# Optimization experiments

Measured on AMD Instinct MI355X. Metric: run time of the kernel, lower is better.

Reference implementation:

```python
import jax, jax.numpy as jnp
import numpy as np

N_NODES = 100000
M_EDGES = 500000
D = 128
L = 2
LRELU_SLOPE = 0.01
LN_EPS = 1e-5


def layer_norm(x, g, b):
    mu = jnp.mean(x, axis=-1, keepdims=True)
    var = jnp.var(x, axis=-1, keepdims=True)
    return (x - mu) * jax.lax.rsqrt(var + LN_EPS) * g + b


def leaky_relu(x):
    return jnp.where(x >= 0, x, LRELU_SLOPE * x)


def setup_inputs() -> dict:
    key = jax.random.key(0)
    ks = jax.random.split(key, 12)
    s = 1.0 / np.sqrt(D)
    inp = {
        "H": jax.random.normal(ks[0], (N_NODES, D), jnp.float32),
        "E": jax.random.normal(ks[1], (M_EDGES, D), jnp.float32),
        "ht": jax.random.randint(ks[2], (M_EDGES, 2), 0, N_NODES, jnp.int64) if jax.config.jax_enable_x64 else jax.random.randint(ks[2], (M_EDGES, 2), 0, N_NODES).astype(jnp.int32),
        "queries": jax.random.randint(ks[3], (M_EDGES,), 0, 2).astype(jnp.int32),
        # per-layer params stacked on leading L axis
        "W_eu": jax.random.uniform(ks[4], (L, 3 * D, D), jnp.float32, -s, s),
        "b_eu": jnp.zeros((L, D), jnp.float32),
        "ln_e_g": jnp.ones((L, D), jnp.float32),
        "ln_e_b": jnp.zeros((L, D), jnp.float32),
        "W_fwd": jax.random.uniform(ks[5], (L, 2 * D, D), jnp.float32, -s, s),
        "b_fwd": jnp.zeros((L, D), jnp.float32),
        "W_back": jax.random.uniform(ks[6], (L, 2 * D, D), jnp.float32, -s, s),
        "b_back": jnp.zeros((L, D), jnp.float32),
        "ln_h_g": jnp.ones((L, D), jnp.float32),
        "ln_h_b": jnp.zeros((L, D), jnp.float32),
    }
    return inp


def aggregate_messages(ht, messages_fwd, messages_back, n):
    # destinations: fwd msgs go to tails, back msgs go to heads
    msg_dst = jnp.concatenate([ht[:, 1], ht[:, 0]])  # [2m]
    messages = jnp.concatenate([messages_fwd, messages_back], axis=0)  # [2m, d]
    agg = jax.ops.segment_sum(messages, msg_dst, num_segments=n)  # [n, d]
    counts = jax.ops.segment_sum(jnp.ones_like(msg_dst, jnp.float32), msg_dst, num_segments=n)
    # torch yields nan/inf for count-0 nodes; clamp to 1 (0/1 = 0) for stability
    return agg / jnp.maximum(counts, 1.0)[:, None]


def reference(H, E, ht, queries, W_eu, b_eu, ln_e_g, ln_e_b,
              W_fwd, b_fwd, W_back, b_back, ln_h_g, ln_h_b):
    n = H.shape[0]
    for l in range(L):
        # --- EdgeUpdateLayer ---
        head_rep = H[ht[:, 0]]  # [m, d]
        tail_rep = H[ht[:, 1]]  # [m, d]
        triple = jnp.concatenate([head_rep, E, tail_rep], axis=1)  # [m, 3d]
        eu = leaky_relu(triple @ W_eu[l] + b_eu[l])
        E = layer_norm(eu + E, ln_e_g[l], ln_e_b[l])
        # --- MessagePassingLayer ---
        msgs_fwd = jnp.concatenate([H[ht[:, 0]], E], axis=1) @ W_fwd[l] + b_fwd[l]
        msgs_back = jnp.concatenate([H[ht[:, 1]], E], axis=1) @ W_back[l] + b_back[l]
        agg = aggregate_messages(ht, msgs_fwd, msgs_back, n)
        H = layer_norm(leaky_relu(agg) + H, ln_h_g[l], ln_h_b[l])
    return H
```

## Files before the change

### kernel.cpp

```cpp
#include <hip/hip_runtime.h>

#define N_NODES 100000
#define M_EDGES 500000
#define D 128
#define SLOPE 0.01f
#define EPS 1e-5f

typedef __attribute__((ext_vector_type(8))) short bf16x8;
typedef __attribute__((ext_vector_type(4))) float f32x4;
typedef __attribute__((ext_vector_type(4))) unsigned int u32x4;

__device__ __forceinline__ unsigned short f2bf(float f) {
    union { float f; unsigned u; } v; v.f = f;
    unsigned r = v.u + 0x7FFF + ((v.u >> 16) & 1);
    return (unsigned short)(r >> 16);
}
__device__ __forceinline__ float bf2f(unsigned short u) {
    union { unsigned u; float f; } v; v.u = ((unsigned)u) << 16; return v.f;
}
__device__ __forceinline__ u32x4 pack8v(f32x4 a, f32x4 b) {
    u32x4 r;
    r.x = ((unsigned)f2bf(a.y) << 16) | f2bf(a.x);
    r.y = ((unsigned)f2bf(a.w) << 16) | f2bf(a.z);
    r.z = ((unsigned)f2bf(b.y) << 16) | f2bf(b.x);
    r.w = ((unsigned)f2bf(b.w) << 16) | f2bf(b.z);
    return r;
}

__global__ void wconv_kernel(const float* __restrict__ src, unsigned short* __restrict__ dst,
                             int K, int total)
{
    int i = blockIdx.x * 256 + threadIdx.x;
    if (i >= total) return;
    int layer_sz = K * 128;
    int l = i / layer_sz;
    int r = i - l * layer_sz;
    int j    = r & 7;
    int lane = (r >> 3) & 63;
    int nt   = (r >> 9) & 7;
    int kk   = r >> 12;
    int row  = kk * 32 + ((lane >> 4) << 3) + j;
    int col  = nt * 16 + (lane & 15);
    dst[i] = f2bf(src[(size_t)l * layer_sz + row * 128 + col]);
}

__global__ void h2b_kernel(const float* __restrict__ src, unsigned short* __restrict__ dst, int total8)
{
    int i = blockIdx.x * 256 + threadIdx.x;
    if (i >= total8) return;
    f32x4 a = ((const f32x4*)src)[2 * i];
    f32x4 b = ((const f32x4*)src)[2 * i + 1];
    ((u32x4*)dst)[i] = pack8v(a, b);
}

__global__ void count_kernel(const int* __restrict__ ht, int* __restrict__ cnt, int m)
{
    int e = blockIdx.x * 256 + threadIdx.x;
    if (e < m) {
        atomicAdd(&cnt[ht[2 * e]],     1);
        atomicAdd(&cnt[ht[2 * e + 1]], 1);
    }
}

__global__ void scanA_kernel(const int* __restrict__ cnt, int* __restrict__ partial,
                             int* __restrict__ bsum, int n)
{
    __shared__ int tmp[256];
    int t = threadIdx.x, i = blockIdx.x * 256 + t;
    int v = (i < n) ? cnt[i] : 0;
    tmp[t] = v;
    __syncthreads();
    for (int s = 1; s < 256; s <<= 1) {
        int x = (t >= s) ? tmp[t - s] : 0;
        __syncthreads();
        tmp[t] += x;
        __syncthreads();
    }
    if (i < n) partial[i] = tmp[t] - v;
    if (t == 255) bsum[blockIdx.x] = tmp[255];
}

__global__ void scanB_kernel(int* __restrict__ bsum, int nb)
{
    __shared__ int tmp[512];
    int t = threadIdx.x;
    int v = (t < nb) ? bsum[t] : 0;
    tmp[t] = v;
    __syncthreads();
    for (int s = 1; s < 512; s <<= 1) {
        int x = (t >= s) ? tmp[t - s] : 0;
        __syncthreads();
        tmp[t] += x;
        __syncthreads();
    }
    if (t < nb) bsum[t] = tmp[t] - v;
}

__global__ void scanC_kernel(const int* __restrict__ partial, const int* __restrict__ bsum,
                             int* __restrict__ off, int* __restrict__ pos, int n)
{
    int i = blockIdx.x * 256 + threadIdx.x;
    if (i < n) {
        int o = partial[i] + bsum[blockIdx.x];
        off[i] = o;
        pos[i] = o;
    }
    if (i == 0) off[n] = 2 * M_EDGES;
}

__global__ void fill_kernel(const int* __restrict__ ht, int* __restrict__ pos,
                            int* __restrict__ slotF, int* __restrict__ slotB, int m)
{
    int e = blockIdx.x * 256 + threadIdx.x;
    if (e < m) {
        int2 p = ((const int2*)ht)[e];
        slotF[e] = atomicAdd(&pos[p.y], 1);
        slotB[e] = atomicAdd(&pos[p.x], 1);
    }
}

template <bool E_F32, bool WRITE_E>
__global__ __launch_bounds__(64, 2)
void edge_mfma_kernel(const unsigned short* __restrict__ Hb,
                      const float* __restrict__ E0,
                      const unsigned short* __restrict__ Ebf,
                      unsigned short* __restrict__ Eout,
                      const int* __restrict__ ht,
                      const unsigned short* __restrict__ Weu,
                      const unsigned short* __restrict__ Wf,
                      const unsigned short* __restrict__ Wb,
                      const float* __restrict__ beu,
                      const float* __restrict__ lneg, const float* __restrict__ lneb,
                      const float* __restrict__ bfw, const float* __restrict__ bbw,
                      const int* __restrict__ slotF, const int* __restrict__ slotB,
                      unsigned short* __restrict__ msg)
{
    __shared__ unsigned char en[16384];

    const int ln  = threadIdx.x;
    const int g   = ln >> 4;
    const int c15 = ln & 15;
    const int ew0 = blockIdx.x * 64;

    int eL = ew0 + ln; if (eL >= M_EDGES) eL = M_EDGES - 1;
    const int slotFv = slotF[eL];
    const int slotBv = slotB[eL];

#pragma unroll
    for (int it = 0; it < 16; ++it) {
        int lin = it * 1024 + ln * 16;
        int row = lin >> 8;
        int e   = ew0 + row;
        int es  = (e < M_EDGES) ? e : (M_EDGES - 1);
        int elem = (lin & 255) >> 1;
        u32x4 pk;
        if (E_F32) {
            const float* s = E0 + (size_t)es * D + elem;
            pk = pack8v(*(const f32x4*)s, *(const f32x4*)(s + 4));
        } else {
            pk = *(const u32x4*)(Ebf + (size_t)es * D + elem);
        }
        *(u32x4*)(en + (lin ^ ((row & 7) << 4))) = pk;
    }

    const unsigned short* hrow[4];
    const unsigned short* trow[4];
    int ebase[4];
#pragma unroll
    for (int m = 0; m < 4; ++m) {
        int e = ew0 + m * 16 + c15;
        int es = (e < M_EDGES) ? e : (M_EDGES - 1);
        int2 p = ((const int2*)ht)[es];
        hrow[m] = Hb + (size_t)p.x * D;
        trow[m] = Hb + (size_t)p.y * D;
        ebase[m] = (m * 16 + c15) * 256 + g * 16;
    }
    const int swz = (c15 & 7) << 4;

    f32x4 acc[4][8];

#pragma unroll
    for (int m = 0; m < 4; ++m)
#pragma unroll
        for (int nt = 0; nt < 8; ++nt) acc[m][nt] = (f32x4){0.f, 0.f, 0.f, 0.f};

    {
        const u32x4* Wg = (const u32x4*)Weu;
        u32x4 bc[8];
        bf16x8 a[4], an[4];
#pragma unroll
        for (int nt = 0; nt < 8; ++nt) bc[nt] = Wg[nt * 64 + ln];
#pragma unroll
        for (int m = 0; m < 4; ++m) a[m] = *(const bf16x8*)(hrow[m] + g * 8);
#pragma unroll 1
        for (int kk = 0; kk < 12; ++kk) {
            if (kk < 11) {
                int kn = kk + 1;
#pragma unroll
                for (int m = 0; m < 4; ++m) {
                    bf16x8 v;
                    if (kn < 4)      v = *(const bf16x8*)(hrow[m] + kn * 32 + g * 8);
                    else if (kn < 8) v = *(const bf16x8*)(en + ((ebase[m] + (kn - 4) * 64) ^ swz));
                    else             v = *(const bf16x8*)(trow[m] + (kn - 8) * 32 + g * 8);
                    an[m] = v;
                }
            }
#pragma unroll
            for (int nt = 0; nt < 8; ++nt) {
                bf16x8 b = *(const bf16x8*)&bc[nt];
#pragma unroll
                for (int m = 0; m < 4; ++m)
                    acc[m][nt] = __builtin_amdgcn_mfma_f32_16x16x32_bf16(a[m], b, acc[m][nt], 0, 0, 0);
                if (kk < 11) bc[nt] = Wg[(kk + 1) * 512 + nt * 64 + ln];
            }
#pragma unroll
            for (int m = 0; m < 4; ++m) a[m] = an[m];
        }
    }

    {
        float be[8], lg[8], lb[8];
#pragma unroll
        for (int nt = 0; nt < 8; ++nt) {
            be[nt] = beu[nt * 16 + c15];
            lg[nt] = lneg[nt * 16 + c15];
            lb[nt] = lneb[nt * 16 + c15];
        }
#pragma unroll
        for (int m = 0; m < 4; ++m) {
            float s[4] = {0.f,0.f,0.f,0.f}, ss[4] = {0.f,0.f,0.f,0.f};
#pragma unroll
            for (int nt = 0; nt < 8; ++nt) {
#pragma unroll
                for (int r = 0; r < 4; ++r) {
                    int row = m * 16 + g * 4 + r;
                    float x = acc[m][nt][r] + be[nt];
                    x = (x >= 0.f) ? x : SLOPE * x;
                    int lin = row * 256 + (nt * 16 + c15) * 2;
                    x += bf2f(*(const unsigned short*)(en + (lin ^ ((row & 7) << 4))));
                    acc[m][nt][r] = x;
                    s[r] += x; ss[r] += x * x;
                }
            }
#pragma unroll
            for (int d = 1; d < 16; d <<= 1) {
#pragma unroll
                for (int r = 0; r < 4; ++r) {
                    s[r]  += __shfl_xor(s[r],  d);
                    ss[r] += __shfl_xor(ss[r], d);
                }
            }
            float mu[4], rs[4];
#pragma unroll
            for (int r = 0; r < 4; ++r) {
                mu[r] = s[r] * (1.0f / 128.0f);
                float var = ss[r] * (1.0f / 128.0f) - mu[r] * mu[r];
                rs[r] = rsqrtf(var + EPS);
            }
#pragma unroll
            for (int nt = 0; nt < 8; ++nt) {
#pragma unroll
                for (int r = 0; r < 4; ++r) {
                    int row = m * 16 + g * 4 + r;
                    float xn = (acc[m][nt][r] - mu[r]) * rs[r] * lg[nt] + lb[nt];
                    int lin = row * 256 + (nt * 16 + c15) * 2;
                    *(unsigned short*)(en + (lin ^ ((row & 7) << 4))) = f2bf(xn);
                }
            }
        }
    }

    if (WRITE_E) {
#pragma unroll
        for (int it = 0; it < 16; ++it) {
            int lin = it * 1024 + ln * 16;
            int row = lin >> 8;
            int e   = ew0 + row;
            if (e < M_EDGES)
                *(u32x4*)(Eout + (size_t)e * D + ((lin & 255) >> 1)) =
                    *(const u32x4*)(en + (lin ^ ((row & 7) << 4)));
        }
    }

#pragma unroll 1
    for (int pass = 0; pass < 2; ++pass) {
        const u32x4* Wg = (const u32x4*)(pass == 0 ? Wf : Wb);
        const unsigned short* ar[4];
#pragma unroll
        for (int m = 0; m < 4; ++m) ar[m] = (pass == 0) ? hrow[m] : trow[m];
#pragma unroll
        for (int m = 0; m < 4; ++m)
#pragma unroll
            for (int nt = 0; nt < 8; ++nt) acc[m][nt] = (f32x4){0.f, 0.f, 0.f, 0.f};

        {
            u32x4 bc[8];
            bf16x8 a[4], an[4];
#pragma unroll
            for (int nt = 0; nt < 8; ++nt) bc[nt] = Wg[nt * 64 + ln];
#pragma unroll
            for (int m = 0; m < 4; ++m) a[m] = *(const bf16x8*)(ar[m] + g * 8);
#pragma unroll 1
            for (int kk = 0; kk < 8; ++kk) {
                if (kk < 7) {
                    int kn = kk + 1;
#pragma unroll
                    for (int m = 0; m < 4; ++m) {
                        bf16x8 v;
                        if (kn < 4) v = *(const bf16x8*)(ar[m] + kn * 32 + g * 8);
                        else        v = *(const bf16x8*)(en + ((ebase[m] + (kn - 4) * 64) ^ swz));
                        an[m] = v;
                    }
                }
#pragma unroll
                for (int nt = 0; nt < 8; ++nt) {
                    bf16x8 b = *(const bf16x8*)&bc[nt];
#pragma unroll
                    for (int m = 0; m < 4; ++m)
                        acc[m][nt] = __builtin_amdgcn_mfma_f32_16x16x32_bf16(a[m], b, acc[m][nt], 0, 0, 0);
                    if (kk < 7) bc[nt] = Wg[(kk + 1) * 512 + nt * 64 + ln];
                }
#pragma unroll
                for (int m = 0; m < 4; ++m) a[m] = an[m];
            }
        }

        {
            const float* bias = (pass == 0) ? bfw : bbw;
            const int slotv = (pass == 0) ? slotFv : slotBv;
            float bv[8];
#pragma unroll
            for (int nt = 0; nt < 8; ++nt) bv[nt] = bias[nt * 16 + c15];
#pragma unroll
            for (int m = 0; m < 4; ++m) {
#pragma unroll
                for (int r = 0; r < 4; ++r) {
                    int erow = m * 16 + g * 4 + r;
                    bool val = (ew0 + erow < M_EDGES);
                    int slot = __shfl(slotv, erow);
                    unsigned* base = (unsigned*)(msg + (size_t)slot * D + (c15 & ~1));
#pragma unroll
                    for (int nt = 0; nt < 8; ++nt) {
                        float v = acc[m][nt][r] + bv[nt];
                        float o = __shfl_xor(v, 1);
                        float lo = (ln & 1) ? o : v;
                        float hi = (ln & 1) ? v : o;
                        unsigned pk = ((unsigned)f2bf(hi) << 16) | f2bf(lo);
                        if (val && ((ln & 1) == (nt >> 2)))
                            base[nt * 8] = pk;
                    }
                }
            }
        }
    }
}

__global__ __launch_bounds__(256)
void node_kernel(const float* __restrict__ Hin, const unsigned short* __restrict__ msg,
                 const int* __restrict__ off, const float* __restrict__ g,
                 const float* __restrict__ b, float* __restrict__ Hout,
                 unsigned short* __restrict__ Hb, int n)
{
    const int wave = threadIdx.x >> 6, lane = threadIdx.x & 63;
    const int node = blockIdx.x * 4 + wave;
    if (node >= n) return;

    const int beg = off[node], end = off[node + 1];
    const float inv = 1.0f / fmaxf((float)(end - beg), 1.0f);
    const unsigned* mb = (const unsigned*)msg;

    float a0 = 0.f, a1 = 0.f;
    int i = beg;
    for (; i + 1 < end; i += 2) {
        unsigned v0 = mb[(size_t)i * 64 + lane];
        unsigned v1 = mb[(size_t)(i + 1) * 64 + lane];
        a0 += bf2f((unsigned short)(v0 & 0xffff)) + bf2f((unsigned short)(v1 & 0xffff));
        a1 += bf2f((unsigned short)(v0 >> 16))    + bf2f((unsigned short)(v1 >> 16));
    }
    if (i < end) {
        unsigned v0 = mb[(size_t)i * 64 + lane];
        a0 += bf2f((unsigned short)(v0 & 0xffff));
        a1 += bf2f((unsigned short)(v0 >> 16));
    }

    a0 *= inv; a1 *= inv;
    a0 = (a0 >= 0.f) ? a0 : SLOPE * a0;
    a1 = (a1 >= 0.f) ? a1 : SLOPE * a1;

    size_t base = (size_t)node * D + 2 * lane;
    float x0 = a0 + Hin[base];
    float x1 = a1 + Hin[base + 1];

    float s = x0 + x1, ss = x0 * x0 + x1 * x1;
#pragma unroll
    for (int d = 1; d < 64; d <<= 1) {
        s  += __shfl_xor(s, d);
        ss += __shfl_xor(ss, d);
    }
    float mu  = s * (1.0f / 128.0f);
    float var = ss * (1.0f / 128.0f) - mu * mu;
    float rs  = rsqrtf(var + EPS);

    float o0 = (x0 - mu) * rs * g[2 * lane]     + b[2 * lane];
    float o1 = (x1 - mu) * rs * g[2 * lane + 1] + b[2 * lane + 1];
    Hout[base]     = o0;
    Hout[base + 1] = o1;
    Hb[base]       = f2bf(o0);
    Hb[base + 1]   = f2bf(o1);
}

extern "C" void kernel_launch(void* const* d_in, const int* in_sizes, int n_in,
                              void* d_out, int out_size, void* d_ws, size_t ws_size,
                              hipStream_t stream)
{
    const float* H0   = (const float*)d_in[0];
    const float* E0   = (const float*)d_in[1];
    const int*   ht   = (const int*)d_in[2];
    const float* Weu  = (const float*)d_in[4];
    const float* beu  = (const float*)d_in[5];
    const float* lneg = (const float*)d_in[6];
    const float* lneb = (const float*)d_in[7];
    const float* Wf   = (const float*)d_in[8];
    const float* bfw  = (const float*)d_in[9];
    const float* Wb   = (const float*)d_in[10];
    const float* bbw  = (const float*)d_in[11];
    const float* lnhg = (const float*)d_in[12];
    const float* lnhb = (const float*)d_in[13];

    float* Hout = (float*)d_out;

    char* ws = (char*)d_ws;
    unsigned short* msg    = (unsigned short*)(ws);
    unsigned short* Ebuf   = (unsigned short*)(ws + 256000000);
    unsigned short* Hb     = (unsigned short*)(ws + 384000000);
    unsigned short* Weu_sw = (unsigned short*)(ws + 409600000);
    unsigned short* Wf_sw  = (unsigned short*)(ws + 409796608);
    unsigned short* Wb_sw  = (unsigned short*)(ws + 409927680);
    int*            cnt    = (int*)(ws + 410058752);
    int*            partial= (int*)(ws + 410458752);
    int*            bsum   = (int*)(ws + 410858752);
    int*            off    = (int*)(ws + 410860800);
    int*            pos    = (int*)(ws + 411260816);
    int*            slotF  = (int*)(ws + 411660816);
    int*            slotB  = (int*)(ws + 413660816);

    wconv_kernel<<<(2*384*128 + 255)/256, 256, 0, stream>>>(Weu, Weu_sw, 384, 2*384*128);
    wconv_kernel<<<(2*256*128 + 255)/256, 256, 0, stream>>>(Wf,  Wf_sw,  256, 2*256*128);
    wconv_kernel<<<(2*256*128 + 255)/256, 256, 0, stream>>>(Wb,  Wb_sw,  256, 2*256*128);
    h2b_kernel<<<(N_NODES * D / 8 + 255)/256, 256, 0, stream>>>(H0, Hb, N_NODES * D / 8);

    const int nscan = (N_NODES + 255) / 256;
    hipMemsetAsync(cnt, 0, (size_t)N_NODES * sizeof(int), stream);
    count_kernel<<<(M_EDGES + 255) / 256, 256, 0, stream>>>(ht, cnt, M_EDGES);
    scanA_kernel<<<nscan, 256, 0, stream>>>(cnt, partial, bsum, N_NODES);
    scanB_kernel<<<1, 512, 0, stream>>>(bsum, nscan);
    scanC_kernel<<<nscan, 256, 0, stream>>>(partial, bsum, off, pos, N_NODES);
    fill_kernel<<<(M_EDGES + 255) / 256, 256, 0, stream>>>(ht, pos, slotF, slotB, M_EDGES);

    const int eblocks = (M_EDGES + 63) / 64;

    for (int l = 0; l < 2; ++l) {
        const float* Hin = (l == 0) ? H0 : Hout;

        if (l == 0) {
            edge_mfma_kernel<true, true><<<eblocks, 64, 0, stream>>>(
                Hb, E0, nullptr, Ebuf, ht,
                Weu_sw, Wf_sw, Wb_sw,
                beu, lneg, lneb, bfw, bbw, slotF, slotB, msg);
        } else {
            edge_mfma_kernel<false, false><<<eblocks, 64, 0, stream>>>(
                Hb, nullptr, Ebuf, nullptr, ht,
                Weu_sw + 49152, Wf_sw + 32768, Wb_sw + 32768,
                beu + D, lneg + D, lneb + D, bfw + D, bbw + D, slotF, slotB, msg);
        }

        node_kernel<<<(N_NODES + 3) / 4, 256, 0, stream>>>(
            Hin, msg, off, lnhg + (size_t)l * D, lnhb + (size_t)l * D, Hout, Hb, N_NODES);
    }
}
```

Measured before the change: 848.8 us.

## Share weight tiles across four waves via double-buffered LDS staging

The edge kernel now runs 256-thread blocks covering 128 edges, with each wave owning 32 edges instead of 64. Weight k-slices are loaded cooperatively into a double-buffered LDS stage with __syncthreads, so one block shares each weight fetch instead of every wave reading weights from global/L2 separately. The next stage's weights, including the Wf/Wb prefetch across phases, are loaded into registers while MFMAs run. This lowers weight traffic and per-wave accumulator registers, but adds block-level barriers and 64KB of LDS per block, which may limit occupancy.

```diff
diff --git a/kernel.cpp b/kernel.cpp
--- a/kernel.cpp
+++ b/kernel.cpp
@@ -120,7 +120,7 @@
 }
 
 template <bool E_F32, bool WRITE_E>
-__global__ __launch_bounds__(64, 2)
+__global__ __launch_bounds__(256, 2)
 void edge_mfma_kernel(const unsigned short* __restrict__ Hb,
                       const float* __restrict__ E0,
                       const unsigned short* __restrict__ Ebf,
@@ -135,22 +135,26 @@
                       const int* __restrict__ slotF, const int* __restrict__ slotB,
                       unsigned short* __restrict__ msg)
 {
-    __shared__ unsigned char en[16384];
-
-    const int ln  = threadIdx.x;
+    __shared__ unsigned char en[32768];
+    __shared__ unsigned char wst[2][16384];
+
+    const int tid = threadIdx.x;
+    const int wv  = tid >> 6;
+    const int ln  = tid & 63;
     const int g   = ln >> 4;
     const int c15 = ln & 15;
-    const int ew0 = blockIdx.x * 64;
-
-    int eL = ew0 + ln; if (eL >= M_EDGES) eL = M_EDGES - 1;
-    const int slotFv = slotF[eL];
-    const int slotBv = slotB[eL];
-
-#pragma unroll
-    for (int it = 0; it < 16; ++it) {
-        int lin = it * 1024 + ln * 16;
+    const int e0  = blockIdx.x * 128;
+    const int ewv = e0 + wv * 32;
+
+    int eS = ewv + (ln & 31); if (eS >= M_EDGES) eS = M_EDGES - 1;
+    const int slotFv = slotF[eS];
+    const int slotBv = slotB[eS];
+
+#pragma unroll
+    for (int it = 0; it < 8; ++it) {
+        int lin = wv * 8192 + it * 1024 + ln * 16;
         int row = lin >> 8;
-        int e   = ew0 + row;
+        int e   = e0 + row;
         int es  = (e < M_EDGES) ? e : (M_EDGES - 1);
         int elem = (lin & 255) >> 1;
         u32x4 pk;
@@ -163,60 +167,73 @@
         *(u32x4*)(en + (lin ^ ((row & 7) << 4))) = pk;
     }
 
-    const unsigned short* hrow[4];
-    const unsigned short* trow[4];
-    int ebase[4];
-#pragma unroll
-    for (int m = 0; m < 4; ++m) {
-        int e = ew0 + m * 16 + c15;
+    const unsigned short* hrow[2];
+    const unsigned short* trow[2];
+    int ebase[2];
+#pragma unroll
+    for (int m = 0; m < 2; ++m) {
+        int e = ewv + m * 16 + c15;
         int es = (e < M_EDGES) ? e : (M_EDGES - 1);
         int2 p = ((const int2*)ht)[es];
         hrow[m] = Hb + (size_t)p.x * D;
         trow[m] = Hb + (size_t)p.y * D;
-        ebase[m] = (m * 16 + c15) * 256 + g * 16;
+        ebase[m] = (wv * 32 + m * 16 + c15) * 256 + g * 16;
     }
     const int swz = (c15 & 7) << 4;
 
-    f32x4 acc[4][8];
-
-#pragma unroll
-    for (int m = 0; m < 4; ++m)
+    f32x4 acc[2][8];
+    u32x4 wreg[4];
+
+#pragma unroll
+    for (int m = 0; m < 2; ++m)
 #pragma unroll
         for (int nt = 0; nt < 8; ++nt) acc[m][nt] = (f32x4){0.f, 0.f, 0.f, 0.f};
 
+    const u32x4* Wg1 = (const u32x4*)Weu;
     {
-        const u32x4* Wg = (const u32x4*)Weu;
-        u32x4 bc[8];
-        bf16x8 a[4], an[4];
-#pragma unroll
-        for (int nt = 0; nt < 8; ++nt) bc[nt] = Wg[nt * 64 + ln];
-#pragma unroll
-        for (int m = 0; m < 4; ++m) a[m] = *(const bf16x8*)(hrow[m] + g * 8);
+#pragma unroll
+        for (int r = 0; r < 4; ++r) wreg[r] = Wg1[r * 256 + tid];
+#pragma unroll
+        for (int r = 0; r < 4; ++r)
+            *(u32x4*)(&wst[0][0] + (r * 256 + tid) * 16) = wreg[r];
+        int cur = 0;
 #pragma unroll 1
-        for (int kk = 0; kk < 12; ++kk) {
-            if (kk < 11) {
-                int kn = kk + 1;
-#pragma unroll
-                for (int m = 0; m < 4; ++m) {
-                    bf16x8 v;
-                    if (kn < 4)      v = *(const bf16x8*)(hrow[m] + kn * 32 + g * 8);
-                    else if (kn < 8) v = *(const bf16x8*)(en + ((ebase[m] + (kn - 4) * 64) ^ swz));
-                    else             v = *(const bf16x8*)(trow[m] + (kn - 8) * 32 + g * 8);
-                    an[m] = v;
-                }
-            }
-#pragma unroll
-            for (int nt = 0; nt < 8; ++nt) {
-                bf16x8 b = *(const bf16x8*)&bc[nt];
-#pragma unroll
-                for (int m = 0; m < 4; ++m)
-                    acc[m][nt] = __builtin_amdgcn_mfma_f32_16x16x32_bf16(a[m], b, acc[m][nt], 0, 0, 0);
-                if (kk < 11) bc[nt] = Wg[(kk + 1) * 512 + nt * 64 + ln];
-            }
-#pragma unroll
-            for (int m = 0; m < 4; ++m) a[m] = an[m];
-        }
-    }
+        for (int s = 0; s < 6; ++s) {
+            if (s < 5) {
+#pragma unroll
+                for (int r = 0; r < 4; ++r) wreg[r] = Wg1[(s + 1) * 1024 + r * 256 + tid];
+            }
+            __syncthreads();
+#pragma unroll
+            for (int k2 = 0; k2 < 2; ++k2) {
+                int kk = s * 2 + k2;
+                bf16x8 a[2];
+#pragma unroll
+                for (int m = 0; m < 2; ++m) {
+                    if (kk < 4)      a[m] = *(const bf16x8*)(hrow[m] + kk * 32 + g * 8);
+                    else if (kk < 8) a[m] = *(const bf16x8*)(en + ((ebase[m] + (kk - 4) * 64) ^ swz));
+                    else             a[m] = *(const bf16x8*)(trow[m] + (kk - 8) * 32 + g * 8);
+                }
+#pragma unroll
+                for (int nt = 0; nt < 8; ++nt) {
+                    bf16x8 b = *(const bf16x8*)(&wst[0][0] + cur * 16384 + (k2 * 8 + nt) * 1024 + ln * 16);
+#pragma unroll
+                    for (int m = 0; m < 2; ++m)
+                        acc[m][nt] = __builtin_amdgcn_mfma_f32_16x16x32_bf16(a[m], b, acc[m][nt], 0, 0, 0);
+                }
+            }
+            if (s < 5) {
+#pragma unroll
+                for (int r = 0; r < 4; ++r)
+                    *(u32x4*)(&wst[0][0] + (cur ^ 1) * 16384 + (r * 256 + tid) * 16) = wreg[r];
+            }
+            cur ^= 1;
+        }
+    }
+
+    const u32x4* Wg2 = (const u32x4*)Wf;
+#pragma unroll
+    for (int r = 0; r < 4; ++r) wreg[r] = Wg2[r * 256 + tid];
 
     {
         float be[8], lg[8], lb[8];
@@ -227,13 +244,13 @@
             lb[nt] = lneb[nt * 16 + c15];
         }
 #pragma unroll
-        for (int m = 0; m < 4; ++m) {
+        for (int m = 0; m < 2; ++m) {
             float s[4] = {0.f,0.f,0.f,0.f}, ss[4] = {0.f,0.f,0.f,0.f};
 #pragma unroll
             for (int nt = 0; nt < 8; ++nt) {
 #pragma unroll
                 for (int r = 0; r < 4; ++r) {
-                    int row = m * 16 + g * 4 + r;
+                    int row = wv * 32 + m * 16 + g * 4 + r;
                     float x = acc[m][nt][r] + be[nt];
                     x = (x >= 0.f) ? x : SLOPE * x;
                     int lin = row * 256 + (nt * 16 + c15) * 2;
@@ -261,7 +278,7 @@
             for (int nt = 0; nt < 8; ++nt) {
 #pragma unroll
                 for (int r = 0; r < 4; ++r) {
-                    int row = m * 16 + g * 4 + r;
+                    int row = wv * 32 + m * 16 + g * 4 + r;
                     float xn = (acc[m][nt][r] - mu[r]) * rs[r] * lg[nt] + lb[nt];
                     int lin = row * 256 + (nt * 16 + c15) * 2;
                     *(unsigned short*)(en + (lin ^ ((row & 7) << 4))) = f2bf(xn);
@@ -272,10 +289,10 @@
 
     if (WRITE_E) {
 #pragma unroll
-        for (int it = 0; it < 16; ++it) {
-            int lin = it * 1024 + ln * 16;
+        for (int it = 0; it < 8; ++it) {
+            int lin = wv * 8192 + it * 1024 + ln * 16;
             int row = lin >> 8;
-            int e   = ew0 + row;
+            int e   = e0 + row;
             if (e < M_EDGES)
                 *(u32x4*)(Eout + (size_t)e * D + ((lin & 255) >> 1)) =
                     *(const u32x4*)(en + (lin ^ ((row & 7) << 4)));
@@ -284,59 +301,67 @@
 
 #pragma unroll 1
     for (int pass = 0; pass < 2; ++pass) {
-        const u32x4* Wg = (const u32x4*)(pass == 0 ? Wf : Wb);
-        const unsigned short* ar[4];
-#pragma unroll
-        for (int m = 0; m < 4; ++m) ar[m] = (pass == 0) ? hrow[m] : trow[m];
-#pragma unroll
-        for (int m = 0; m < 4; ++m)
+        const u32x4* Wg = pass ? (const u32x4*)Wb : Wg2;
+        const unsigned short* ar[2];
+        ar[0] = pass ? trow[0] : hrow[0];
+        ar[1] = pass ? trow[1] : hrow[1];
+#pragma unroll
+        for (int m = 0; m < 2; ++m)
 #pragma unroll
             for (int nt = 0; nt < 8; ++nt) acc[m][nt] = (f32x4){0.f, 0.f, 0.f, 0.f};
 
+#pragma unroll
+        for (int r = 0; r < 4; ++r)
+            *(u32x4*)(&wst[0][0] + (r * 256 + tid) * 16) = wreg[r];
+        int cur = 0;
+#pragma unroll 1
+        for (int s = 0; s < 4; ++s) {
+            if (s < 3) {
+#pragma unroll
+                for (int r = 0; r < 4; ++r) wreg[r] = Wg[(s + 1) * 1024 + r * 256 + tid];
+            } else if (pass == 0) {
+                const u32x4* Wg3 = (const u32x4*)Wb;
+#pragma unroll
+                for (int r = 0; r < 4; ++r) wreg[r] = Wg3[r * 256 + tid];
+            }
+            __syncthreads();
+#pragma unroll
+            for (int k2 = 0; k2 < 2; ++k2) {
+                int kk = s * 2 + k2;
+                bf16x8 a[2];
+#pragma unroll
+                for (int m = 0; m < 2; ++m) {
+                    if (kk < 4) a[m] = *(const bf16x8*)(ar[m] + kk * 32 + g * 8);
+                    else        a[m] = *(const bf16x8*)(en + ((ebase[m] + (kk - 4) * 64) ^ swz));
+                }
+#pragma unroll
+                for (int nt = 0; nt < 8; ++nt) {
+                    bf16x8 b = *(const bf16x8*)(&wst[0][0] + cur * 16384 + (k2 * 8 + nt) * 1024 + ln * 16);
+#pragma unroll
+                    for (int m = 0; m < 2; ++m)
+                        acc[m][nt] = __builtin_amdgcn_mfma_f32_16x16x32_bf16(a[m], b, acc[m][nt], 0, 0, 0);
+                }
+            }
+            if (s < 3) {
+#pragma unroll
+                for (int r = 0; r < 4; ++r)
+                    *(u32x4*)(&wst[0][0] + (cur ^ 1) * 16384 + (r * 256 + tid) * 16) = wreg[r];
+            }
+            cur ^= 1;
+        }
+
         {
-            u32x4 bc[8];
-            bf16x8 a[4], an[4];
-#pragma unroll
-            for (int nt = 0; nt < 8; ++nt) bc[nt] = Wg[nt * 64 + ln];
-#pragma unroll
-            for (int m = 0; m < 4; ++m) a[m] = *(const bf16x8*)(ar[m] + g * 8);
-#pragma unroll 1
-            for (int kk = 0; kk < 8; ++kk) {
-                if (kk < 7) {
-                    int kn = kk + 1;
-#pragma unroll
-                    for (int m = 0; m < 4; ++m) {
-                        bf16x8 v;
-                        if (kn < 4) v = *(const bf16x8*)(ar[m] + kn * 32 + g * 8);
-                        else        v = *(const bf16x8*)(en + ((ebase[m] + (kn - 4) * 64) ^ swz));
-                        an[m] = v;
-                    }
-                }
-#pragma unroll
-                for (int nt = 0; nt < 8; ++nt) {
-                    bf16x8 b = *(const bf16x8*)&bc[nt];
-#pragma unroll
-                    for (int m = 0; m < 4; ++m)
-                        acc[m][nt] = __builtin_amdgcn_mfma_f32_16x16x32_bf16(a[m], b, acc[m][nt], 0, 0, 0);
-                    if (kk < 7) bc[nt] = Wg[(kk + 1) * 512 + nt * 64 + ln];
-                }
-#pragma unroll
-                for (int m = 0; m < 4; ++m) a[m] = an[m];
-            }
-        }
-
-        {
-            const float* bias = (pass == 0) ? bfw : bbw;
-            const int slotv = (pass == 0) ? slotFv : slotBv;
+            const float* bias = pass ? bbw : bfw;
+            const int slotv = pass ? slotBv : slotFv;
             float bv[8];
 #pragma unroll
             for (int nt = 0; nt < 8; ++nt) bv[nt] = bias[nt * 16 + c15];
 #pragma unroll
-            for (int m = 0; m < 4; ++m) {
+            for (int m = 0; m < 2; ++m) {
 #pragma unroll
                 for (int r = 0; r < 4; ++r) {
                     int erow = m * 16 + g * 4 + r;
-                    bool val = (ew0 + erow < M_EDGES);
+                    bool val = (ewv + erow < M_EDGES);
                     int slot = __shfl(slotv, erow);
                     unsigned* base = (unsigned*)(msg + (size_t)slot * D + (c15 & ~1));
 #pragma unroll
@@ -457,18 +482,18 @@
     scanC_kernel<<<nscan, 256, 0, stream>>>(partial, bsum, off, pos, N_NODES);
     fill_kernel<<<(M_EDGES + 255) / 256, 256, 0, stream>>>(ht, pos, slotF, slotB, M_EDGES);
 
-    const int eblocks = (M_EDGES + 63) / 64;
+    const int eblocks = (M_EDGES + 127) / 128;
 
     for (int l = 0; l < 2; ++l) {
         const float* Hin = (l == 0) ? H0 : Hout;
 
         if (l == 0) {
-            edge_mfma_kernel<true, true><<<eblocks, 64, 0, stream>>>(
+            edge_mfma_kernel<true, true><<<eblocks, 256, 0, stream>>>(
                 Hb, E0, nullptr, Ebuf, ht,
                 Weu_sw, Wf_sw, Wb_sw,
                 beu, lneg, lneb, bfw, bbw, slotF, slotB, msg);
         } else {
-            edge_mfma_kernel<false, false><<<eblocks, 64, 0, stream>>>(
+            edge_mfma_kernel<false, false><<<eblocks, 256, 0, stream>>>(
                 Hb, nullptr, Ebuf, nullptr, ht,
                 Weu_sw + 49152, Wf_sw + 32768, Wb_sw + 32768,
                 beu + D, lneg + D, lneb + D, bfw + D, bbw + D, slotF, slotB, msg);
```

Measured after the change: 855.8 us. About the same (+0.8%).
